# Performance work log

Hardware: AMD Instinct MI355X
Metric: run time of the kernel (lower is better)

The kernel has to match this reference:

```python
import jax, jax.numpy as jnp
import numpy as np

N = 100_000      # nodes
E = 1_600_000    # edges (before self-loops)
IN, OUT, HID = 64, 32, 64
BN_EPS = 1e-5

def _mlp(h, w1, b1, g, beta, w2, b2):
    # PyG MLP (num_layers=2, plain_last=True): Linear -> BatchNorm(train) -> ReLU -> Linear
    h = h @ w1 + b1
    mu = jnp.mean(h, axis=0)
    var = jnp.var(h, axis=0)
    h = (h - mu) * jax.lax.rsqrt(var + BN_EPS) * g + beta
    return jax.nn.relu(h) @ w2 + b2

def setup_inputs() -> dict:
    key = jax.random.key(0)
    ks = jax.random.split(key, 12)
    def rn(k, shape):
        fan_in = shape[0]
        return jax.random.normal(k, shape, jnp.float32) / np.sqrt(fan_in)
    x = jax.random.normal(ks[0], (N, IN), jnp.float32)
    pos = jax.random.normal(ks[1], (N, 3), jnp.float32)
    edge_index = jax.random.randint(ks[2], (2, E), 0, N, jnp.int64)
    return {
        "x": x, "pos": pos, "edge_index": edge_index,
        "w_lin": rn(ks[3], (IN, OUT)), "w_src": rn(ks[4], (IN, OUT)), "w_dst": rn(ks[5], (IN, OUT)),
        "pos_w1": rn(ks[6], (3, HID)), "pos_b1": jnp.zeros((HID,), jnp.float32),
        "pos_g": jnp.ones((HID,), jnp.float32), "pos_beta": jnp.zeros((HID,), jnp.float32),
        "pos_w2": rn(ks[7], (HID, OUT)), "pos_b2": jnp.zeros((OUT,), jnp.float32),
        "att_w1": rn(ks[8], (OUT, HID)), "att_b1": jnp.zeros((HID,), jnp.float32),
        "att_g": jnp.ones((HID,), jnp.float32), "att_beta": jnp.zeros((HID,), jnp.float32),
        "att_w2": rn(ks[9], (HID, OUT)), "att_b2": jnp.zeros((OUT,), jnp.float32),
    }

def reference(x, pos, edge_index, w_lin, w_src, w_dst,
              pos_w1, pos_b1, pos_g, pos_beta, pos_w2, pos_b2,
              att_w1, att_b1, att_g, att_beta, att_w2, att_b2):
    n = x.shape[0]
    # add self-loops (PointTransformerConv default add_self_loops=True)
    loops = jnp.arange(n, dtype=edge_index.dtype)
    src = jnp.concatenate([edge_index[0], loops])  # j (message source)
    dst = jnp.concatenate([edge_index[1], loops])  # i (message target)

    alpha_src = x @ w_src          # [N, OUT]
    alpha_dst = x @ w_dst          # [N, OUT]
    x_val = x @ w_lin              # [N, OUT]

    delta = _mlp(pos[dst] - pos[src], pos_w1, pos_b1, pos_g, pos_beta, pos_w2, pos_b2)  # [E', OUT]
    a = _mlp(alpha_dst[dst] - alpha_src[src] + delta, att_w1, att_b1, att_g, att_beta, att_w2, att_b2)

    # per-destination-node, per-channel softmax over incoming edges
    a_max = jax.ops.segment_max(a, dst, num_segments=n)           # [N, OUT]
    a = jnp.exp(a - a_max[dst])
    denom = jax.ops.segment_sum(a, dst, num_segments=n)           # [N, OUT]
    a = a / (denom[dst] + 1e-16)

    msg = a * (x_val[src] + delta)                                # [E', OUT]
    out = jax.ops.segment_sum(msg, dst, num_segments=n)           # [N, OUT]
    return out
```

## Files before the change

### kernel.cpp

```cpp
#include <hip/hip_runtime.h>

typedef unsigned int uint;
typedef unsigned short ushort;

#define BN_EPS 1e-5f

using bf16x8 = __attribute__((ext_vector_type(8))) short;
using f32x16 = __attribute__((ext_vector_type(16))) float;

union FragU { uint w[4]; bf16x8 v; };

__device__ __forceinline__ uint pk2(float lo, float hi) {
    uint r;
    asm("v_cvt_pk_bf16_f32 %0, %1, %2" : "=v"(r) : "v"(lo), "v"(hi));
    return r;
}
__device__ __forceinline__ float bfu_lo(uint u) { return __uint_as_float(u << 16); }
__device__ __forceinline__ float bfu_hi(uint u) { return __uint_as_float(u & 0xffff0000u); }

__device__ __forceinline__ float upk(const uint* p, int idx) {
    uint u = p[idx >> 1];
    return (idx & 1) ? bfu_hi(u) : bfu_lo(u);
}
__device__ __forceinline__ float upq(const uint2* gq, int r) {
    int g = r >> 2, j = r & 3;
    uint u = (j < 2) ? gq[g].x : gq[g].y;
    return (j & 1) ? bfu_hi(u) : bfu_lo(u);
}

__device__ __forceinline__ void get_rowmap(int col, int* rowv) {
    FragU pa, pb;
    float c = (float)col;
    #pragma unroll
    for (int j = 0; j < 4; j++) { pa.w[j] = pk2(c, c); pb.w[j] = pk2(1.f, 1.f); }
    f32x16 d;
    #pragma unroll
    for (int r = 0; r < 16; r++) d[r] = 0.f;
    d = __builtin_amdgcn_mfma_f32_32x32x16_bf16(pa.v, pb.v, d, 0, 0, 0);
    #pragma unroll
    for (int r = 0; r < 16; r++) {
        int m = (int)(d[r] * 0.0625f + 0.5f);
        rowv[r] = (m < 0) ? 0 : (m > 31 ? 31 : m);
    }
}

template<bool SORTED>
__device__ __forceinline__ void edge_sd(int e, const int* __restrict__ ei,
                                        const int* __restrict__ srcs,
                                        const int* __restrict__ dsts,
                                        int nE, int& src, int& dst) {
    if (SORTED) { src = srcs[e]; dst = dsts[e]; }
    else if (e < nE) { src = ei[e]; dst = ei[nE + e]; }
    else { src = e - nE; dst = src; }
}

__global__ __launch_bounds__(256) void k_node_lin(
    const float* __restrict__ x,
    const float* __restrict__ w_src, const float* __restrict__ w_dst,
    const float* __restrict__ w_lin,
    uint* __restrict__ asx, uint* __restrict__ aDb,
    int nNodes)
{
    int n = blockIdx.x * 256 + threadIdx.x;
    if (n >= nNodes) return;
    float xr[64];
    const float4* xp = (const float4*)(x + (size_t)n * 64);
    #pragma unroll
    for (int i = 0; i < 16; i++) {
        float4 v = xp[i];
        xr[4*i] = v.x; xr[4*i+1] = v.y; xr[4*i+2] = v.z; xr[4*i+3] = v.w;
    }
    const float* ws[3] = { w_src, w_lin, w_dst };
    uint* outs[3] = { asx + (size_t)n*32, asx + (size_t)n*32 + 16, aDb + (size_t)n*16 };
    #pragma unroll
    for (int m = 0; m < 3; m++) {
        const float* w = ws[m];
        float acc[32];
        #pragma unroll
        for (int o = 0; o < 32; o++) acc[o] = 0.f;
        #pragma unroll
        for (int k = 0; k < 64; k++) {
            float xk = xr[k];
            #pragma unroll
            for (int o = 0; o < 32; o++) acc[o] = fmaf(xk, w[k*32+o], acc[o]);
        }
        uint4* op = (uint4*)outs[m];
        #pragma unroll
        for (int q = 0; q < 4; q++) {
            uint4 v;
            v.x = pk2(acc[8*q+0], acc[8*q+1]);
            v.y = pk2(acc[8*q+2], acc[8*q+3]);
            v.z = pk2(acc[8*q+4], acc[8*q+5]);
            v.w = pk2(acc[8*q+6], acc[8*q+7]);
            op[q] = v;
        }
    }
}

__global__ __launch_bounds__(256) void k_pos4(
    const float* __restrict__ pos, float4* __restrict__ pos4, int n)
{
    int i = blockIdx.x * 256 + threadIdx.x;
    if (i < n) pos4[i] = make_float4(pos[i*3], pos[i*3+1], pos[i*3+2], 0.f);
}

__global__ __launch_bounds__(256) void k_hist(
    const int* __restrict__ ei, int* __restrict__ cnt, int nE, int eTot)
{
    int e = blockIdx.x * 256 + threadIdx.x;
    if (e >= eTot) return;
    int dst = (e < nE) ? ei[nE + e] : (e - nE);
    atomicAdd(&cnt[dst], 1);
}

#define SCH 1024
__global__ __launch_bounds__(256) void k_scan1(
    const int* __restrict__ cnt, int* __restrict__ cur,
    int* __restrict__ blkS, int n)
{
    __shared__ int ls[256];
    int t = threadIdx.x;
    int base = blockIdx.x * SCH + t * 4;
    int v0 = (base+0 < n) ? cnt[base+0] : 0;
    int v1 = (base+1 < n) ? cnt[base+1] : 0;
    int v2 = (base+2 < n) ? cnt[base+2] : 0;
    int v3 = (base+3 < n) ? cnt[base+3] : 0;
    int tsum = v0 + v1 + v2 + v3;
    ls[t] = tsum;
    __syncthreads();
    for (int o = 1; o < 256; o <<= 1) {
        int x = (t >= o) ? ls[t-o] : 0;
        __syncthreads();
        ls[t] += x;
        __syncthreads();
    }
    if (t == 255) blkS[blockIdx.x] = ls[255];
    int run = ls[t] - tsum;
    if (base+0 < n) cur[base+0] = run; run += v0;
    if (base+1 < n) cur[base+1] = run; run += v1;
    if (base+2 < n) cur[base+2] = run; run += v2;
    if (base+3 < n) cur[base+3] = run;
}

__global__ void k_scan2(const int* __restrict__ blkS, int* __restrict__ blkOff, int nb)
{
    __shared__ int ls[256];
    int t = threadIdx.x;
    int v = (t < nb) ? blkS[t] : 0;
    ls[t] = v;
    __syncthreads();
    for (int o = 1; o < 256; o <<= 1) {
        int x = (t >= o) ? ls[t-o] : 0;
        __syncthreads();
        ls[t] += x;
        __syncthreads();
    }
    if (t < nb) blkOff[t] = ls[t] - v;
}

__global__ __launch_bounds__(256) void k_scan3(
    int* __restrict__ cur, const int* __restrict__ blkOff, int n)
{
    int off = blkOff[blockIdx.x];
    int base = blockIdx.x * SCH + threadIdx.x * 4;
    #pragma unroll
    for (int j = 0; j < 4; j++) {
        int i = base + j;
        if (i < n) cur[i] += off;
    }
}

__global__ __launch_bounds__(256) void k_rank(
    const int* __restrict__ ei, int* __restrict__ cur,
    int* __restrict__ srcs, int* __restrict__ dsts, int nE, int eTot)
{
    int e = blockIdx.x * 256 + threadIdx.x;
    if (e >= eTot) return;
    int src, dst;
    if (e < nE) { src = ei[e]; dst = ei[nE + e]; }
    else        { src = e - nE; dst = src; }
    int slot = atomicAdd(&cur[dst], 1);
    srcs[slot] = src; dsts[slot] = dst;
}

__global__ __launch_bounds__(256) void k_pos_mom(
    const int* __restrict__ ei, const float4* __restrict__ pos4,
    float* __restrict__ partM, int nE)
{
    float m[9];
    #pragma unroll
    for (int c = 0; c < 9; c++) m[c] = 0.f;
    int stride = gridDim.x * blockDim.x;
    for (int e = blockIdx.x * blockDim.x + threadIdx.x; e < nE; e += stride) {
        int src = ei[e], dst = ei[nE + e];
        float4 pd = pos4[dst], ps = pos4[src];
        float d0 = pd.x - ps.x, d1 = pd.y - ps.y, d2 = pd.z - ps.z;
        m[0] += d0; m[1] += d1; m[2] += d2;
        m[3] = fmaf(d0,d0,m[3]); m[4] = fmaf(d0,d1,m[4]); m[5] = fmaf(d0,d2,m[5]);
        m[6] = fmaf(d1,d1,m[6]); m[7] = fmaf(d1,d2,m[7]); m[8] = fmaf(d2,d2,m[8]);
    }
    __shared__ float red[4][9];
    int w = threadIdx.x >> 6;
    #pragma unroll
    for (int c = 0; c < 9; c++) {
        float t = m[c];
        for (int o = 32; o > 0; o >>= 1) t += __shfl_down(t, o, 64);
        if ((threadIdx.x & 63) == 0) red[w][c] = t;
    }
    __syncthreads();
    if (threadIdx.x < 9)
        partM[blockIdx.x * 9 + threadIdx.x] =
            red[0][threadIdx.x] + red[1][threadIdx.x] + red[2][threadIdx.x] + red[3][threadIdx.x];
}

__global__ void k_bn1_mom(const float* __restrict__ partM, int nBlk,
                          const float* __restrict__ pw1, const float* __restrict__ pb1,
                          const float* __restrict__ g, const float* __restrict__ beta,
                          float* __restrict__ bn, float invE)
{
    __shared__ float mom_s[9];
    int l = threadIdx.x;
    #pragma unroll
    for (int c = 0; c < 9; c++) {
        float s = 0.f;
        for (int i = l; i < nBlk; i += 64) s += partM[i*9 + c];
        for (int o = 32; o > 0; o >>= 1) s += __shfl_down(s, o, 64);
        if (l == 0) mom_s[c] = s;
    }
    __syncthreads();
    int c = l;
    if (c < 64) {
        float w0 = pw1[c], w1 = pw1[64+c], w2 = pw1[128+c], b = pb1[c];
        float S = fmaf(w0, mom_s[0], fmaf(w1, mom_s[1], w2 * mom_s[2]));
        float Q = w0*w0*mom_s[3] + 2.f*w0*w1*mom_s[4] + 2.f*w0*w2*mom_s[5]
                + w1*w1*mom_s[6] + 2.f*w1*w2*mom_s[7] + w2*w2*mom_s[8];
        float mu  = S * invE + b;
        float E2  = Q * invE + 2.f * b * (S * invE) + b * b;
        float var = fmaxf(E2 - mu * mu, 0.f);
        float sc  = rsqrtf(var + BN_EPS) * g[c];
        bn[c]      = sc;
        bn[64+c]   = beta[c] - mu * sc;
    }
}

__global__ __launch_bounds__(256) void k_red_stats(
    const float* __restrict__ partD, float* __restrict__ stats2, int nBlk)
{
    int c = blockIdx.x;
    float s = 0.f;
    for (int i = threadIdx.x; i < nBlk; i += 256) s += partD[(size_t)i*128 + c];
    for (int o = 32; o > 0; o >>= 1) s += __shfl_down(s, o, 64);
    __shared__ float red[4];
    if ((threadIdx.x & 63) == 0) red[threadIdx.x >> 6] = s;
    __syncthreads();
    if (threadIdx.x == 0) stats2[c] = red[0] + red[1] + red[2] + red[3];
}

__global__ void k_bn_fin(const float* __restrict__ stats,
                         const float* __restrict__ g, const float* __restrict__ beta,
                         const float* __restrict__ bias,
                         float* __restrict__ bn, float inv_ep)
{
    int c = threadIdx.x;
    if (c < 64) {
        float b   = bias ? bias[c] : 0.f;
        float m0  = stats[c] * inv_ep;
        float mu  = m0 + b;
        float eq  = stats[64+c] * inv_ep + 2.f*b*m0 + b*b;
        float var = fmaxf(eq - mu * mu, 0.f);
        float sc  = rsqrtf(var + BN_EPS) * g[c];
        bn[c]      = sc;
        bn[64+c]   = beta[c] - mu * sc;
    }
}

__global__ void k_fold1(const float* __restrict__ pw1, const float* __restrict__ pb1,
                        const float* __restrict__ bn1,
                        float* __restrict__ pw1f, float* __restrict__ pb1f)
{
    int i = threadIdx.x;
    if (i < 192) pw1f[i] = pw1[i] * bn1[i & 63];
    if (i < 64)  pb1f[i] = pb1[i] * bn1[i] + bn1[64 + i];
}

__global__ void k_fold2(const float* __restrict__ aw1, const float* __restrict__ ab1,
                        const float* __restrict__ bn2,
                        float* __restrict__ aw1f, float* __restrict__ ab1f)
{
    int i = blockIdx.x * 256 + threadIdx.x;
    if (i < 2048) aw1f[i] = aw1[i] * bn2[i & 63];
    if (i < 64)   ab1f[i] = ab1[i] * bn2[i] + bn2[64 + i];
}

template<bool SORTED>
__global__ __launch_bounds__(256, 2) void k_delta_stats(
    const int* __restrict__ ei, const int* __restrict__ srcs, const int* __restrict__ dsts,
    const float4* __restrict__ pos4,
    const uint* __restrict__ asx, const uint* __restrict__ aDb,
    const float* __restrict__ pw1f, const float* __restrict__ pb1f,
    const float* __restrict__ pw2, const float* __restrict__ pb2,
    const float* __restrict__ aw1,
    float* __restrict__ partD, int nE, int eTot)
{
    const int lane = threadIdx.x & 63;
    const int col  = lane & 31;
    const int h    = lane >> 5;
    const int wid  = threadIdx.x >> 6;

    __shared__ float redS[4][64], redQ[4][64];
    __shared__ uint sbuf[4][1024];
    {
        int w = threadIdx.x >> 6, c = threadIdx.x & 63;
        redS[w][c] = 0.f; redQ[w][c] = 0.f;
    }

    bool quadOK;
    int q2[4];
    FragU fw_pw2[4];
    FragU fw_aw1[2][2];
    uint pb2p[8];
    {
        int rowv[16];
        get_rowmap(col, rowv);
        quadOK = true;
        #pragma unroll
        for (int g = 0; g < 4; g++)
            quadOK = quadOK && (rowv[4*g+1] == rowv[4*g]+1)
                            && (rowv[4*g+2] == rowv[4*g]+2)
                            && (rowv[4*g+3] == rowv[4*g]+3);
        #pragma unroll
        for (int g = 0; g < 4; g++) q2[g] = rowv[4*g] >> 2;
        #pragma unroll
        for (int kt = 0; kt < 4; kt++)
            #pragma unroll
            for (int jw = 0; jw < 4; jw++) {
                int m = 2*jw;
                int c0 = 16*kt + 8*(m>>2) + 4*h + (m&3);
                fw_pw2[kt].w[jw] = pk2(pw2[c0*32 + col], pw2[(c0+1)*32 + col]);
            }
        #pragma unroll
        for (int mt = 0; mt < 2; mt++)
            #pragma unroll
            for (int kt = 0; kt < 2; kt++)
                #pragma unroll
                for (int jw = 0; jw < 4; jw++) {
                    int u0 = rowv[8*kt + 2*jw], u1 = rowv[8*kt + 2*jw + 1];
                    fw_aw1[mt][kt].w[jw] = pk2(aw1[u0*64 + 32*mt + col],
                                               aw1[u1*64 + 32*mt + col]);
                }
        #pragma unroll
        for (int g = 0; g < 8; g++)
            pb2p[g] = pk2(pb2[rowv[2*g]], pb2[rowv[2*g+1]]);
    }

    float sA[32], qA[32];
    #pragma unroll
    for (int i = 0; i < 32; i++) { sA[i] = 0.f; qA[i] = 0.f; }

    const int nT = (eTot + 31) >> 5;
    const int gw = (blockIdx.x << 2) + (threadIdx.x >> 6);
    const int nW = gridDim.x << 2;

    if (quadOK) {
        for (int t = gw; t < nT; t += nW) {
            int e = t*32 + col;
            bool valid = e < eTot;
            int ec = valid ? e : eTot - 1;
            int src, dst;
            edge_sd<SORTED>(ec, ei, srcs, dsts, nE, src, dst);
            #pragma unroll
            for (int it = 0; it < 4; it++) {
                int j  = it*8 + (lane >> 3);
                int sj = __shfl(src, j, 64);
                int w  = lane & 7;
                uint4 v = *(const uint4*)(asx + (size_t)sj*32 + w*4);
                *(uint4*)&sbuf[wid][j*32 + ((w ^ (j & 7)) << 2)] = v;
            }
            float4 ps = pos4[src], pd = pos4[dst];
            uint2 gd2[4];
            {
                const uint* rd = aDb + (size_t)dst*16;
                #pragma unroll
                for (int g = 0; g < 4; g++) gd2[g] = *(const uint2*)(rd + 2*q2[g]);
            }
            float p0 = pd.x - ps.x, p1 = pd.y - ps.y, p2 = pd.z - ps.z;

            FragU ft[4];
            #pragma unroll
            for (int kt = 0; kt < 4; kt++)
                #pragma unroll
                for (int mm = 0; mm < 2; mm++) {
                    int cb = 16*kt + 8*mm + 4*h;
                    float4 w0 = *(const float4*)(pw1f +       cb);
                    float4 w1 = *(const float4*)(pw1f + 64  + cb);
                    float4 w2 = *(const float4*)(pw1f + 128 + cb);
                    float4 bb = *(const float4*)(pb1f + cb);
                    float t0 = fmaxf(fmaf(p0,w0.x, fmaf(p1,w1.x, fmaf(p2,w2.x, bb.x))), 0.f);
                    float t1 = fmaxf(fmaf(p0,w0.y, fmaf(p1,w1.y, fmaf(p2,w2.y, bb.y))), 0.f);
                    float t2 = fmaxf(fmaf(p0,w0.z, fmaf(p1,w1.z, fmaf(p2,w2.z, bb.z))), 0.f);
                    float t3 = fmaxf(fmaf(p0,w0.w, fmaf(p1,w1.w, fmaf(p2,w2.w, bb.w))), 0.f);
                    ft[kt].w[2*mm+0] = pk2(t0, t1);
                    ft[kt].w[2*mm+1] = pk2(t2, t3);
                }
            f32x16 adl;
            #pragma unroll
            for (int r = 0; r < 16; r++) adl[r] = upk(pb2p, r);
            #pragma unroll
            for (int kt = 0; kt < 4; kt++)
                adl = __builtin_amdgcn_mfma_f32_32x32x16_bf16(fw_pw2[kt].v, ft[kt].v, adl, 0, 0, 0);

            uint2 gs2[4];
            #pragma unroll
            for (int g = 0; g < 4; g++) {
                int wq = q2[g] >> 1, hf = (q2[g] & 1) << 1;
                gs2[g] = *(const uint2*)&sbuf[wid][col*32 + ((wq ^ (col & 7)) << 2) + hf];
            }

            FragU fu[2];
            #pragma unroll
            for (int kt = 0; kt < 2; kt++)
                #pragma unroll
                for (int jw = 0; jw < 4; jw++) {
                    int r0 = 8*kt + 2*jw;
                    fu[kt].w[jw] = pk2(adl[r0]   + upq(gd2, r0)   - upq(gs2, r0),
                                       adl[r0+1] + upq(gd2, r0+1) - upq(gs2, r0+1));
                }

            f32x16 ah0, ah1;
            #pragma unroll
            for (int r = 0; r < 16; r++) { ah0[r] = 0.f; ah1[r] = 0.f; }
            #pragma unroll
            for (int kt = 0; kt < 2; kt++) {
                ah0 = __builtin_amdgcn_mfma_f32_32x32x16_bf16(fw_aw1[0][kt].v, fu[kt].v, ah0, 0, 0, 0);
                ah1 = __builtin_amdgcn_mfma_f32_32x32x16_bf16(fw_aw1[1][kt].v, fu[kt].v, ah1, 0, 0, 0);
            }
            if (valid) {
                #pragma unroll
                for (int r = 0; r < 16; r++) {
                    sA[r]    += ah0[r];
                    qA[r]     = fmaf(ah0[r], ah0[r], qA[r]);
                    sA[16+r] += ah1[r];
                    qA[16+r]  = fmaf(ah1[r], ah1[r], qA[16+r]);
                }
            }
        }
    } else {
        int rowv[16];
        get_rowmap(col, rowv);
        for (int t = gw; t < nT; t += nW) {
            int e = t*32 + col;
            bool valid = e < eTot;
            int ec = valid ? e : eTot - 1;
            int src, dst;
            edge_sd<SORTED>(ec, ei, srcs, dsts, nE, src, dst);
            float4 pd = pos4[dst], ps = pos4[src];
            float p0 = pd.x - ps.x, p1 = pd.y - ps.y, p2 = pd.z - ps.z;
            FragU ft[4];
            #pragma unroll
            for (int kt = 0; kt < 4; kt++)
                #pragma unroll
                for (int mm = 0; mm < 2; mm++) {
                    int cb = 16*kt + 8*mm + 4*h;
                    float4 w0 = *(const float4*)(pw1f +       cb);
                    float4 w1 = *(const float4*)(pw1f + 64  + cb);
                    float4 w2 = *(const float4*)(pw1f + 128 + cb);
                    float4 bb = *(const float4*)(pb1f + cb);
                    float t0 = fmaxf(fmaf(p0,w0.x, fmaf(p1,w1.x, fmaf(p2,w2.x, bb.x))), 0.f);
                    float t1 = fmaxf(fmaf(p0,w0.y, fmaf(p1,w1.y, fmaf(p2,w2.y, bb.y))), 0.f);
                    float t2 = fmaxf(fmaf(p0,w0.z, fmaf(p1,w1.z, fmaf(p2,w2.z, bb.z))), 0.f);
                    float t3 = fmaxf(fmaf(p0,w0.w, fmaf(p1,w1.w, fmaf(p2,w2.w, bb.w))), 0.f);
                    ft[kt].w[2*mm+0] = pk2(t0, t1);
                    ft[kt].w[2*mm+1] = pk2(t2, t3);
                }
            f32x16 adl;
            #pragma unroll
            for (int r = 0; r < 16; r++) adl[r] = upk(pb2p, r);
            #pragma unroll
            for (int kt = 0; kt < 4; kt++)
                adl = __builtin_amdgcn_mfma_f32_32x32x16_bf16(fw_pw2[kt].v, ft[kt].v, adl, 0, 0, 0);
            const ushort* rs = (const ushort*)(asx + (size_t)src*32);
            const ushort* rd = (const ushort*)(aDb + (size_t)dst*16);
            FragU fu[2];
            #pragma unroll
            for (int kt = 0; kt < 2; kt++)
                #pragma unroll
                for (int jw = 0; jw < 4; jw++) {
                    int r0 = 8*kt + 2*jw;
                    float u0 = adl[r0]   + __uint_as_float(((uint)rd[rowv[r0]])   << 16)
                                         - __uint_as_float(((uint)rs[rowv[r0]])   << 16);
                    float u1 = adl[r0+1] + __uint_as_float(((uint)rd[rowv[r0+1]]) << 16)
                                         - __uint_as_float(((uint)rs[rowv[r0+1]]) << 16);
                    fu[kt].w[jw] = pk2(u0, u1);
                }
            f32x16 ah0, ah1;
            #pragma unroll
            for (int r = 0; r < 16; r++) { ah0[r] = 0.f; ah1[r] = 0.f; }
            #pragma unroll
            for (int kt = 0; kt < 2; kt++) {
                ah0 = __builtin_amdgcn_mfma_f32_32x32x16_bf16(fw_aw1[0][kt].v, fu[kt].v, ah0, 0, 0, 0);
                ah1 = __builtin_amdgcn_mfma_f32_32x32x16_bf16(fw_aw1[1][kt].v, fu[kt].v, ah1, 0, 0, 0);
            }
            if (valid) {
                #pragma unroll
                for (int r = 0; r < 16; r++) {
                    sA[r]    += ah0[r];
                    qA[r]     = fmaf(ah0[r], ah0[r], qA[r]);
                    sA[16+r] += ah1[r];
                    qA[16+r]  = fmaf(ah1[r], ah1[r], qA[16+r]);
                }
            }
        }
    }

    __syncthreads();
    {
        int rv[16];
        get_rowmap(col, rv);
        int w = threadIdx.x >> 6;
        #pragma unroll
        for (int idx = 0; idx < 32; idx++) {
            float vs = sA[idx], vq = qA[idx];
            for (int off = 16; off > 0; off >>= 1) {
                vs += __shfl_xor(vs, off, 64);
                vq += __shfl_xor(vq, off, 64);
            }
            if ((threadIdx.x & 31) == 0) {
                int mt = idx >> 4, r = idx & 15;
                int c = 32*mt + rv[r];
                redS[w][c] = vs;
                redQ[w][c] = vq;
            }
        }
    }
    __syncthreads();
    if (threadIdx.x < 64) {
        int c = threadIdx.x;
        float S = redS[0][c] + redS[1][c] + redS[2][c] + redS[3][c];
        float Q = redQ[0][c] + redQ[1][c] + redQ[2][c] + redQ[3][c];
        partD[(size_t)blockIdx.x*128 + c]      = S;
        partD[(size_t)blockIdx.x*128 + 64 + c] = Q;
    }
}

template<bool SORTED>
__global__ __launch_bounds__(256, 2) void k_att_agg(
    const int* __restrict__ ei, const int* __restrict__ srcs, const int* __restrict__ dsts,
    const float4* __restrict__ pos4,
    const uint* __restrict__ asx, const uint* __restrict__ aDb,
    const float* __restrict__ pw1f, const float* __restrict__ pb1f,
    const float* __restrict__ pw2, const float* __restrict__ pb2,
    const float* __restrict__ aw1f, const float* __restrict__ ab1f,
    const float* __restrict__ aw2, const float* __restrict__ ab2,
    float* __restrict__ denom, float* __restrict__ outp,
    int nE, int eTot)
{
    const int lane = threadIdx.x & 63;
    const int col  = lane & 31;
    const int h    = lane >> 5;
    const int wid  = threadIdx.x >> 6;

    __shared__ uint sbuf[4][1024];

    bool quadOK;
    int q2[4];
    FragU fw_pw2[4], fw_aw2[4];
    FragU fw_aw1[2][2];
    uint pb2p[8], ab2p[8], ab1p[16];
    {
        int rowv[16];
        get_rowmap(col, rowv);
        quadOK = true;
        #pragma unroll
        for (int g = 0; g < 4; g++)
            quadOK = quadOK && (rowv[4*g+1] == rowv[4*g]+1)
                            && (rowv[4*g+2] == rowv[4*g]+2)
                            && (rowv[4*g+3] == rowv[4*g]+3);
        #pragma unroll
        for (int g = 0; g < 4; g++) q2[g] = rowv[4*g] >> 2;
        #pragma unroll
        for (int kt = 0; kt < 4; kt++)
            #pragma unroll
            for (int jw = 0; jw < 4; jw++) {
                int m = 2*jw;
                int c0 = 16*kt + 8*(m>>2) + 4*h + (m&3);
                fw_pw2[kt].w[jw] = pk2(pw2[c0*32 + col], pw2[(c0+1)*32 + col]);
                int o0 = 32*(kt>>1) + rowv[8*(kt&1) + m];
                int o1 = 32*(kt>>1) + rowv[8*(kt&1) + m + 1];
                fw_aw2[kt].w[jw] = pk2(aw2[o0*32 + col], aw2[o1*32 + col]);
            }
        #pragma unroll
        for (int mt = 0; mt < 2; mt++)
            #pragma unroll
            for (int kt = 0; kt < 2; kt++)
                #pragma unroll
                for (int jw = 0; jw < 4; jw++) {
                    int u0 = rowv[8*kt + 2*jw], u1 = rowv[8*kt + 2*jw + 1];
                    fw_aw1[mt][kt].w[jw] = pk2(aw1f[u0*64 + 32*mt + col],
                                               aw1f[u1*64 + 32*mt + col]);
                }
        #pragma unroll
        for (int g = 0; g < 8; g++) {
            pb2p[g] = pk2(pb2[rowv[2*g]], pb2[rowv[2*g+1]]);
            ab2p[g] = pk2(ab2[rowv[2*g]], ab2[rowv[2*g+1]]);
            ab1p[g]     = pk2(ab1f[rowv[2*g]],      ab1f[rowv[2*g+1]]);
            ab1p[8 + g] = pk2(ab1f[32 + rowv[2*g]], ab1f[32 + rowv[2*g+1]]);
        }
    }

    const int nT = (eTot + 31) >> 5;
    const int gw = (blockIdx.x << 2) + (threadIdx.x >> 6);
    const int nW = gridDim.x << 2;

    if (quadOK) {
        for (int t = gw; t < nT; t += nW) {
            int e = t*32 + col;
            bool valid = e < eTot;
            int ec = valid ? e : eTot - 1;
            int src, dst;
            edge_sd<SORTED>(ec, ei, srcs, dsts, nE, src, dst);
            #pragma unroll
            for (int it = 0; it < 4; it++) {
                int j  = it*8 + (lane >> 3);
                int sj = __shfl(src, j, 64);
                int w  = lane & 7;
                uint4 v = *(const uint4*)(asx + (size_t)sj*32 + w*4);
                *(uint4*)&sbuf[wid][j*32 + ((w ^ (j & 7)) << 2)] = v;
            }
            float4 ps = pos4[src], pd = pos4[dst];
            uint2 gd2[4];
            {
                const uint* rd = aDb + (size_t)dst*16;
                #pragma unroll
                for (int g = 0; g < 4; g++) gd2[g] = *(const uint2*)(rd + 2*q2[g]);
            }
            float p0 = pd.x - ps.x, p1 = pd.y - ps.y, p2 = pd.z - ps.z;

            FragU ft[4];
            #pragma unroll
            for (int kt = 0; kt < 4; kt++)
                #pragma unroll
                for (int mm = 0; mm < 2; mm++) {
                    int cb = 16*kt + 8*mm + 4*h;
                    float4 w0 = *(const float4*)(pw1f +       cb);
                    float4 w1 = *(const float4*)(pw1f + 64  + cb);
                    float4 w2 = *(const float4*)(pw1f + 128 + cb);
                    float4 bb = *(const float4*)(pb1f + cb);
                    float t0 = fmaxf(fmaf(p0,w0.x, fmaf(p1,w1.x, fmaf(p2,w2.x, bb.x))), 0.f);
                    float t1 = fmaxf(fmaf(p0,w0.y, fmaf(p1,w1.y, fmaf(p2,w2.y, bb.y))), 0.f);
                    float t2 = fmaxf(fmaf(p0,w0.z, fmaf(p1,w1.z, fmaf(p2,w2.z, bb.z))), 0.f);
                    float t3 = fmaxf(fmaf(p0,w0.w, fmaf(p1,w1.w, fmaf(p2,w2.w, bb.w))), 0.f);
                    ft[kt].w[2*mm+0] = pk2(t0, t1);
                    ft[kt].w[2*mm+1] = pk2(t2, t3);
                }
            f32x16 adl;
            #pragma unroll
            for (int r = 0; r < 16; r++) adl[r] = upk(pb2p, r);
            #pragma unroll
            for (int kt = 0; kt < 4; kt++)
                adl = __builtin_amdgcn_mfma_f32_32x32x16_bf16(fw_pw2[kt].v, ft[kt].v, adl, 0, 0, 0);

            uint2 gs2[4], gx2[4];
            #pragma unroll
            for (int g = 0; g < 4; g++) {
                int wq = q2[g] >> 1, hf = (q2[g] & 1) << 1;
                gs2[g] = *(const uint2*)&sbuf[wid][col*32 + ((wq ^ (col & 7)) << 2) + hf];
                gx2[g] = *(const uint2*)&sbuf[wid][col*32 + (((4 + wq) ^ (col & 7)) << 2) + hf];
            }

            FragU fu[2];
            #pragma unroll
            for (int kt = 0; kt < 2; kt++)
                #pragma unroll
                for (int jw = 0; jw < 4; jw++) {
                    int r0 = 8*kt + 2*jw;
                    fu[kt].w[jw] = pk2(adl[r0]   + upq(gd2, r0)   - upq(gs2, r0),
                                       adl[r0+1] + upq(gd2, r0+1) - upq(gs2, r0+1));
                }

            f32x16 ah0, ah1;
            #pragma unroll
            for (int r = 0; r < 16; r++) { ah0[r] = upk(ab1p, r); ah1[r] = upk(ab1p, 16 + r); }
            #pragma unroll
            for (int kt = 0; kt < 2; kt++) {
                ah0 = __builtin_amdgcn_mfma_f32_32x32x16_bf16(fw_aw1[0][kt].v, fu[kt].v, ah0, 0, 0, 0);
                ah1 = __builtin_amdgcn_mfma_f32_32x32x16_bf16(fw_aw1[1][kt].v, fu[kt].v, ah1, 0, 0, 0);
            }
            FragU fh[4];
            #pragma unroll
            for (int q = 0; q < 4; q++)
                #pragma unroll
                for (int jw = 0; jw < 4; jw++) {
                    int r0 = 8*(q&1) + 2*jw;
                    float x0 = (q < 2) ? ah0[r0]   : ah1[r0];
                    float x1 = (q < 2) ? ah0[r0+1] : ah1[r0+1];
                    fh[q].w[jw] = pk2(fmaxf(x0, 0.f), fmaxf(x1, 0.f));
                }
            f32x16 aa;
            #pragma unroll
            for (int r = 0; r < 16; r++) aa[r] = upk(ab2p, r);
            aa = __builtin_amdgcn_mfma_f32_32x32x16_bf16(fw_aw2[0].v, fh[0].v, aa, 0, 0, 0);
            aa = __builtin_amdgcn_mfma_f32_32x32x16_bf16(fw_aw2[1].v, fh[1].v, aa, 0, 0, 0);
            aa = __builtin_amdgcn_mfma_f32_32x32x16_bf16(fw_aw2[2].v, fh[2].v, aa, 0, 0, 0);
            aa = __builtin_amdgcn_mfma_f32_32x32x16_bf16(fw_aw2[3].v, fh[3].v, aa, 0, 0, 0);

            if (SORTED) {
                int lw = lane & 31;
                int dprev = __shfl_up(dst, 1, 32);
                bool isHead = (lw == 0) || (dprev != dst);
                bool eq1  = (__shfl_down(dst, 1, 32)  == dst) && (lw + 1  < 32);
                bool eq2  = (__shfl_down(dst, 2, 32)  == dst) && (lw + 2  < 32);
                bool eq4  = (__shfl_down(dst, 4, 32)  == dst) && (lw + 4  < 32);
                bool eq8  = (__shfl_down(dst, 8, 32)  == dst) && (lw + 8  < 32);
                bool eq16 = (__shfl_down(dst, 16, 32) == dst) && (lw + 16 < 32);
                float* drow = denom + (size_t)dst * 32;
                float* orow = outp  + (size_t)dst * 32;
                #pragma unroll
                for (int r = 0; r < 16; r++) {
                    float ea = __expf(fminf(aa[r], 35.f));
                    float ev = valid ? ea : 0.f;
                    float mv = valid ? ea * (upq(gx2, r) + adl[r]) : 0.f;
                    { float a = __shfl_down(ev,1,32),  b = __shfl_down(mv,1,32);  if (eq1)  { ev += a; mv += b; } }
                    { float a = __shfl_down(ev,2,32),  b = __shfl_down(mv,2,32);  if (eq2)  { ev += a; mv += b; } }
                    { float a = __shfl_down(ev,4,32),  b = __shfl_down(mv,4,32);  if (eq4)  { ev += a; mv += b; } }
                    { float a = __shfl_down(ev,8,32),  b = __shfl_down(mv,8,32);  if (eq8)  { ev += a; mv += b; } }
                    { float a = __shfl_down(ev,16,32), b = __shfl_down(mv,16,32); if (eq16) { ev += a; mv += b; } }
                    if (isHead) {
                        int o = 4*q2[r>>2] + (r&3);
                        unsafeAtomicAdd(drow + o, ev);
                        unsafeAtomicAdd(orow + o, mv);
                    }
                }
            } else if (valid) {
                float* drow = denom + (size_t)dst * 32;
                float* orow = outp  + (size_t)dst * 32;
                #pragma unroll
                for (int r = 0; r < 16; r++) {
                    int o = 4*q2[r>>2] + (r&3);
                    float ea = __expf(fminf(aa[r], 35.f));
                    unsafeAtomicAdd(drow + o, ea);
                    unsafeAtomicAdd(orow + o, ea * (upq(gx2, r) + adl[r]));
                }
            }
        }
    } else {
        int rowv[16];
        get_rowmap(col, rowv);
        for (int t = gw; t < nT; t += nW) {
            int e = t*32 + col;
            bool valid = e < eTot;
            int ec = valid ? e : eTot - 1;
            int src, dst;
            edge_sd<SORTED>(ec, ei, srcs, dsts, nE, src, dst);
            float4 pd = pos4[dst], ps = pos4[src];
            float p0 = pd.x - ps.x, p1 = pd.y - ps.y, p2 = pd.z - ps.z;
            FragU ft[4];
            #pragma unroll
            for (int kt = 0; kt < 4; kt++)
                #pragma unroll
                for (int mm = 0; mm < 2; mm++) {
                    int cb = 16*kt + 8*mm + 4*h;
                    float4 w0 = *(const float4*)(pw1f +       cb);
                    float4 w1 = *(const float4*)(pw1f + 64  + cb);
                    float4 w2 = *(const float4*)(pw1f + 128 + cb);
                    float4 bb = *(const float4*)(pb1f + cb);
                    float t0 = fmaxf(fmaf(p0,w0.x, fmaf(p1,w1.x, fmaf(p2,w2.x, bb.x))), 0.f);
                    float t1 = fmaxf(fmaf(p0,w0.y, fmaf(p1,w1.y, fmaf(p2,w2.y, bb.y))), 0.f);
                    float t2 = fmaxf(fmaf(p0,w0.z, fmaf(p1,w1.z, fmaf(p2,w2.z, bb.z))), 0.f);
                    float t3 = fmaxf(fmaf(p0,w0.w, fmaf(p1,w1.w, fmaf(p2,w2.w, bb.w))), 0.f);
                    ft[kt].w[2*mm+0] = pk2(t0, t1);
                    ft[kt].w[2*mm+1] = pk2(t2, t3);
                }
            f32x16 adl;
            #pragma unroll
            for (int r = 0; r < 16; r++) adl[r] = upk(pb2p, r);
            #pragma unroll
            for (int kt = 0; kt < 4; kt++)
                adl = __builtin_amdgcn_mfma_f32_32x32x16_bf16(fw_pw2[kt].v, ft[kt].v, adl, 0, 0, 0);
            const ushort* rs = (const ushort*)(asx + (size_t)src*32);
            const ushort* rd = (const ushort*)(aDb + (size_t)dst*16);
            FragU fu[2];
            float xg[16];
            #pragma unroll
            for (int r = 0; r < 16; r++)
                xg[r] = __uint_as_float(((uint)rs[32 + rowv[r]]) << 16);
            #pragma unroll
            for (int kt = 0; kt < 2; kt++)
                #pragma unroll
                for (int jw = 0; jw < 4; jw++) {
                    int r0 = 8*kt + 2*jw;
                    float u0 = adl[r0]   + __uint_as_float(((uint)rd[rowv[r0]])   << 16)
                                         - __uint_as_float(((uint)rs[rowv[r0]])   << 16);
                    float u1 = adl[r0+1] + __uint_as_float(((uint)rd[rowv[r0+1]]) << 16)
                                         - __uint_as_float(((uint)rs[rowv[r0+1]]) << 16);
                    fu[kt].w[jw] = pk2(u0, u1);
                }
            f32x16 ah0, ah1;
            #pragma unroll
            for (int r = 0; r < 16; r++) { ah0[r] = upk(ab1p, r); ah1[r] = upk(ab1p, 16 + r); }
            #pragma unroll
            for (int kt = 0; kt < 2; kt++) {
                ah0 = __builtin_amdgcn_mfma_f32_32x32x16_bf16(fw_aw1[0][kt].v, fu[kt].v, ah0, 0, 0, 0);
                ah1 = __builtin_amdgcn_mfma_f32_32x32x16_bf16(fw_aw1[1][kt].v, fu[kt].v, ah1, 0, 0, 0);
            }
            FragU fh[4];
            #pragma unroll
            for (int q = 0; q < 4; q++)
                #pragma unroll
                for (int jw = 0; jw < 4; jw++) {
                    int r0 = 8*(q&1) + 2*jw;
                    float x0 = (q < 2) ? ah0[r0]   : ah1[r0];
                    float x1 = (q < 2) ? ah0[r0+1] : ah1[r0+1];
                    fh[q].w[jw] = pk2(fmaxf(x0, 0.f), fmaxf(x1, 0.f));
                }
            f32x16 aa;
            #pragma unroll
            for (int r = 0; r < 16; r++) aa[r] = upk(ab2p, r);
            aa = __builtin_amdgcn_mfma_f32_32x32x16_bf16(fw_aw2[0].v, fh[0].v, aa, 0, 0, 0);
            aa = __builtin_amdgcn_mfma_f32_32x32x16_bf16(fw_aw2[1].v, fh[1].v, aa, 0, 0, 0);
            aa = __builtin_amdgcn_mfma_f32_32x32x16_bf16(fw_aw2[2].v, fh[2].v, aa, 0, 0, 0);
            aa = __builtin_amdgcn_mfma_f32_32x32x16_bf16(fw_aw2[3].v, fh[3].v, aa, 0, 0, 0);
            if (SORTED) {
                int lw = lane & 31;
                int dprev = __shfl_up(dst, 1, 32);
                bool isHead = (lw == 0) || (dprev != dst);
                bool eq1  = (__shfl_down(dst, 1, 32)  == dst) && (lw + 1  < 32);
                bool eq2  = (__shfl_down(dst, 2, 32)  == dst) && (lw + 2  < 32);
                bool eq4  = (__shfl_down(dst, 4, 32)  == dst) && (lw + 4  < 32);
                bool eq8  = (__shfl_down(dst, 8, 32)  == dst) && (lw + 8  < 32);
                bool eq16 = (__shfl_down(dst, 16, 32) == dst) && (lw + 16 < 32);
                float* drow = denom + (size_t)dst * 32;
                float* orow = outp  + (size_t)dst * 32;
                #pragma unroll
                for (int r = 0; r < 16; r++) {
                    float ea = __expf(fminf(aa[r], 35.f));
                    float ev = valid ? ea : 0.f;
                    float mv = valid ? ea * (xg[r] + adl[r]) : 0.f;
                    { float a = __shfl_down(ev,1,32),  b = __shfl_down(mv,1,32);  if (eq1)  { ev += a; mv += b; } }
                    { float a = __shfl_down(ev,2,32),  b = __shfl_down(mv,2,32);  if (eq2)  { ev += a; mv += b; } }
                    { float a = __shfl_down(ev,4,32),  b = __shfl_down(mv,4,32);  if (eq4)  { ev += a; mv += b; } }
                    { float a = __shfl_down(ev,8,32),  b = __shfl_down(mv,8,32);  if (eq8)  { ev += a; mv += b; } }
                    { float a = __shfl_down(ev,16,32), b = __shfl_down(mv,16,32); if (eq16) { ev += a; mv += b; } }
                    if (isHead) {
                        int o = rowv[r];
                        unsafeAtomicAdd(drow + o, ev);
                        unsafeAtomicAdd(orow + o, mv);
                    }
                }
            } else if (valid) {
                float* drow = denom + (size_t)dst * 32;
                float* orow = outp  + (size_t)dst * 32;
                #pragma unroll
                for (int r = 0; r < 16; r++) {
                    int o = rowv[r];
                    float ea = __expf(fminf(aa[r], 35.f));
                    unsafeAtomicAdd(drow + o, ea);
                    unsafeAtomicAdd(orow + o, ea * (xg[r] + adl[r]));
                }
            }
        }
    }
}

__global__ __launch_bounds__(256) void k_norm(
    float* __restrict__ out, const float* __restrict__ denom, int total)
{
    int i = blockIdx.x * 256 + threadIdx.x;
    if (i < total) out[i] = out[i] / (denom[i] + 1e-16f);
}

extern "C" void kernel_launch(void* const* d_in, const int* in_sizes, int n_in,
                              void* d_out, int out_size, void* d_ws, size_t ws_size,
                              hipStream_t stream)
{
    const float* x     = (const float*)d_in[0];
    const float* pos   = (const float*)d_in[1];
    const int*   ei    = (const int*)d_in[2];
    const float* w_lin = (const float*)d_in[3];
    const float* w_src = (const float*)d_in[4];
    const float* w_dst = (const float*)d_in[5];
    const float* pw1   = (const float*)d_in[6];
    const float* pb1   = (const float*)d_in[7];
    const float* pg    = (const float*)d_in[8];
    const float* pbeta = (const float*)d_in[9];
    const float* pw2   = (const float*)d_in[10];
    const float* pb2   = (const float*)d_in[11];
    const float* aw1   = (const float*)d_in[12];
    const float* ab1   = (const float*)d_in[13];
    const float* ag    = (const float*)d_in[14];
    const float* abeta = (const float*)d_in[15];
    const float* aw2   = (const float*)d_in[16];
    const float* ab2   = (const float*)d_in[17];
    float* out = (float*)d_out;

    const int nNodes = in_sizes[0] / 64;
    const int nE     = in_sizes[2] / 2;
    const int eTot   = nE + nNodes;

    const int PMBLK = 1024;
    const int DBLK  = 2048;

    const size_t nF = (size_t)nNodes * 32;
    uint*   asx   = (uint*)d_ws;
    uint*   aDb   = asx + (size_t)nNodes*32;
    float*  pos4  = (float*)(aDb + (size_t)nNodes*16);
    float*  denom = pos4 + (size_t)nNodes*4;
    float*  stats = denom + nF;
    float*  bn1   = stats + 512;
    float*  bn2   = bn1 + 128;
    float*  pw1f  = bn2 + 128;
    float*  pb1f  = pw1f + 192;
    float*  aw1f  = pb1f + 64;
    float*  ab1f  = aw1f + 2048;
    float*  partM = ab1f + 64;
    float*  partD = partM + (size_t)PMBLK*9;
    float*  fend  = partD + (size_t)DBLK*128;

    int* cnt    = (int*)fend;
    int* cur    = cnt + nNodes;
    int* blkS   = cur + nNodes;
    int* blkOff = blkS + 256;
    int* srcs   = blkOff + 256;
    int* dsts   = srcs + eTot;

    size_t need_sorted = ((char*)(dsts + eTot)) - ((char*)d_ws);
    const bool sorted = ws_size >= need_sorted;

    const int nb = (nNodes + SCH - 1) / SCH;

    hipMemsetAsync(out,   0, nF * sizeof(float), stream);
    hipMemsetAsync(denom, 0, nF * sizeof(float), stream);

    k_node_lin<<<(nNodes + 255) / 256, 256, 0, stream>>>(
        x, w_src, w_dst, w_lin, asx, aDb, nNodes);
    k_pos4<<<(nNodes + 255) / 256, 256, 0, stream>>>(pos, (float4*)pos4, nNodes);

    k_pos_mom<<<PMBLK, 256, 0, stream>>>(ei, (const float4*)pos4, partM, nE);
    k_bn1_mom<<<1, 64, 0, stream>>>(partM, PMBLK, pw1, pb1, pg, pbeta, bn1,
                                    1.0f / (float)eTot);
    k_fold1<<<1, 256, 0, stream>>>(pw1, pb1, bn1, pw1f, pb1f);

    if (sorted) {
        hipMemsetAsync(cnt, 0, (size_t)nNodes * sizeof(int), stream);
        k_hist<<<(eTot + 255) / 256, 256, 0, stream>>>(ei, cnt, nE, eTot);
        k_scan1<<<nb, 256, 0, stream>>>(cnt, cur, blkS, nNodes);
        k_scan2<<<1, 256, 0, stream>>>(blkS, blkOff, nb);
        k_scan3<<<nb, 256, 0, stream>>>(cur, blkOff, nNodes);
        k_rank<<<(eTot + 255) / 256, 256, 0, stream>>>(ei, cur, srcs, dsts, nE, eTot);

        k_delta_stats<true><<<DBLK, 256, 0, stream>>>(
            ei, srcs, dsts, (const float4*)pos4, asx, aDb,
            pw1f, pb1f, pw2, pb2, aw1, partD, nE, eTot);
        k_red_stats<<<128, 256, 0, stream>>>(partD, stats + 128, DBLK);
        k_bn_fin<<<1, 64, 0, stream>>>(stats + 128, ag, abeta, ab1, bn2, 1.0f / (float)eTot);
        k_fold2<<<8, 256, 0, stream>>>(aw1, ab1, bn2, aw1f, ab1f);
        k_att_agg<true><<<DBLK, 256, 0, stream>>>(
            ei, srcs, dsts, (const float4*)pos4, asx, aDb,
            pw1f, pb1f, pw2, pb2, aw1f, ab1f, aw2, ab2, denom, out, nE, eTot);
    } else {
        k_delta_stats<false><<<DBLK, 256, 0, stream>>>(
            ei, nullptr, nullptr, (const float4*)pos4, asx, aDb,
            pw1f, pb1f, pw2, pb2, aw1, partD, nE, eTot);
        k_red_stats<<<128, 256, 0, stream>>>(partD, stats + 128, DBLK);
        k_bn_fin<<<1, 64, 0, stream>>>(stats + 128, ag, abeta, ab1, bn2, 1.0f / (float)eTot);
        k_fold2<<<8, 256, 0, stream>>>(aw1, ab1, bn2, aw1f, ab1f);
        k_att_agg<false><<<DBLK, 256, 0, stream>>>(
            ei, nullptr, nullptr, (const float4*)pos4, asx, aDb,
            pw1f, pb1f, pw2, pb2, aw1f, ab1f, aw2, ab2, denom, out, nE, eTot);
    }
    k_norm<<<(((int)nF) + 255) / 256, 256, 0, stream>>>(out, denom, (int)nF);
}
```

Baseline: 852.7 us.

## Assign whole destination segments per wave to drop atomics, memsets and normalize pass

In the sorted path, each wave now gets an edge range aligned to destination-segment boundaries, found by a ballot search over the sorted dst array. Partial sums for a segment that spans several 32-edge chunks are carried in shared memory. Each output row is written once, already divided by the softmax denominator, so the atomics, the zeroing memsets and the separate normalize kernel are no longer needed. The cost is a boundary search per wave and possible load imbalance when segments are long. Nodes with no incoming edges now depend on self-loops to get written, since out is no longer zeroed.

```diff
diff --git a/kernel.cpp b/kernel.cpp
--- a/kernel.cpp
+++ b/kernel.cpp
@@ -44,14 +44,25 @@
     }
 }
 
-template<bool SORTED>
-__device__ __forceinline__ void edge_sd(int e, const int* __restrict__ ei,
-                                        const int* __restrict__ srcs,
-                                        const int* __restrict__ dsts,
-                                        int nE, int& src, int& dst) {
-    if (SORTED) { src = srcs[e]; dst = dsts[e]; }
-    else if (e < nE) { src = ei[e]; dst = ei[nE + e]; }
-    else { src = e - nE; dst = src; }
+__device__ __forceinline__ int adj_boundary(const int* __restrict__ dsts,
+                                            long tgt, int eTot, int lane) {
+    if (tgt <= 0) return 0;
+    if (tgt >= eTot) return eTot;
+    long base = tgt;
+    while (base < eTot) {
+        long e = base + lane;
+        bool head;
+        if (e < eTot) head = (dsts[e] != dsts[e - 1]);
+        else          head = true;
+        unsigned long long m = __ballot(head);
+        if (m) {
+            int fl = __ffsll((long long)m) - 1;
+            long r = base + fl;
+            return (r > eTot) ? eTot : (int)r;
+        }
+        base += 64;
+    }
+    return eTot;
 }
 
 __global__ __launch_bounds__(256) void k_node_lin(
@@ -367,7 +378,9 @@
             bool valid = e < eTot;
             int ec = valid ? e : eTot - 1;
             int src, dst;
-            edge_sd<SORTED>(ec, ei, srcs, dsts, nE, src, dst);
+            if (SORTED) { src = srcs[ec]; dst = dsts[ec]; }
+            else if (ec < nE) { src = ei[ec]; dst = ei[nE + ec]; }
+            else { src = ec - nE; dst = src; }
             #pragma unroll
             for (int it = 0; it < 4; it++) {
                 int j  = it*8 + (lane >> 3);
@@ -452,7 +465,9 @@
             bool valid = e < eTot;
             int ec = valid ? e : eTot - 1;
             int src, dst;
-            edge_sd<SORTED>(ec, ei, srcs, dsts, nE, src, dst);
+            if (SORTED) { src = srcs[ec]; dst = dsts[ec]; }
+            else if (ec < nE) { src = ei[ec]; dst = ei[nE + ec]; }
+            else { src = ec - nE; dst = src; }
             float4 pd = pos4[dst], ps = pos4[src];
             float p0 = pd.x - ps.x, p1 = pd.y - ps.y, p2 = pd.z - ps.z;
             FragU ft[4];
@@ -542,10 +557,232 @@
     }
 }
 
-template<bool SORTED>
-__global__ __launch_bounds__(256, 2) void k_att_agg(
-    const int* __restrict__ ei, const int* __restrict__ srcs, const int* __restrict__ dsts,
+__global__ __launch_bounds__(256, 2) void k_att_run(
+    const int* __restrict__ srcs, const int* __restrict__ dsts,
     const float4* __restrict__ pos4,
+    const uint* __restrict__ asx, const uint* __restrict__ aDb,
+    const float* __restrict__ pw1f, const float* __restrict__ pb1f,
+    const float* __restrict__ pw2, const float* __restrict__ pb2,
+    const float* __restrict__ aw1f, const float* __restrict__ ab1f,
+    const float* __restrict__ aw2, const float* __restrict__ ab2,
+    float* __restrict__ outp, int eTot, int nWaves)
+{
+    const int lane = threadIdx.x & 63;
+    const int col  = lane & 31;
+    const int h    = lane >> 5;
+    const int wid  = threadIdx.x >> 6;
+    const int gwid = blockIdx.x * 4 + wid;
+
+    __shared__ uint sbuf[4][1024];
+    __shared__ int   s_cdst[4][2];
+    __shared__ float s_cD[4][2][16], s_cO[4][2][16];
+
+    bool quadOK;
+    int q2[4];
+    int rowv[16];
+    FragU fw_pw2[4], fw_aw2[4];
+    FragU fw_aw1[2][2];
+    uint pb2p[8], ab2p[8], ab1p[16];
+    {
+        get_rowmap(col, rowv);
+        quadOK = true;
+        #pragma unroll
+        for (int g = 0; g < 4; g++)
+            quadOK = quadOK && (rowv[4*g+1] == rowv[4*g]+1)
+                            && (rowv[4*g+2] == rowv[4*g]+2)
+                            && (rowv[4*g+3] == rowv[4*g]+3);
+        #pragma unroll
+        for (int g = 0; g < 4; g++) q2[g] = rowv[4*g] >> 2;
+        #pragma unroll
+        for (int kt = 0; kt < 4; kt++)
+            #pragma unroll
+            for (int jw = 0; jw < 4; jw++) {
+                int m = 2*jw;
+                int c0 = 16*kt + 8*(m>>2) + 4*h + (m&3);
+                fw_pw2[kt].w[jw] = pk2(pw2[c0*32 + col], pw2[(c0+1)*32 + col]);
+                int o0 = 32*(kt>>1) + rowv[8*(kt&1) + m];
+                int o1 = 32*(kt>>1) + rowv[8*(kt&1) + m + 1];
+                fw_aw2[kt].w[jw] = pk2(aw2[o0*32 + col], aw2[o1*32 + col]);
+            }
+        #pragma unroll
+        for (int mt = 0; mt < 2; mt++)
+            #pragma unroll
+            for (int kt = 0; kt < 2; kt++)
+                #pragma unroll
+                for (int jw = 0; jw < 4; jw++) {
+                    int u0 = rowv[8*kt + 2*jw], u1 = rowv[8*kt + 2*jw + 1];
+                    fw_aw1[mt][kt].w[jw] = pk2(aw1f[u0*64 + 32*mt + col],
+                                               aw1f[u1*64 + 32*mt + col]);
+                }
+        #pragma unroll
+        for (int g = 0; g < 8; g++) {
+            pb2p[g] = pk2(pb2[rowv[2*g]], pb2[rowv[2*g+1]]);
+            ab2p[g] = pk2(ab2[rowv[2*g]], ab2[rowv[2*g+1]]);
+            ab1p[g]     = pk2(ab1f[rowv[2*g]],      ab1f[rowv[2*g+1]]);
+            ab1p[8 + g] = pk2(ab1f[32 + rowv[2*g]], ab1f[32 + rowv[2*g+1]]);
+        }
+    }
+
+    long tgt0 = (long)gwid * (long)eTot / (long)nWaves;
+    long tgt1 = (long)(gwid + 1) * (long)eTot / (long)nWaves;
+    int rs = adj_boundary(dsts, tgt0, eTot, lane);
+    int re = adj_boundary(dsts, tgt1, eTot, lane);
+
+    if ((lane & 31) == 0) s_cdst[wid][h] = -1;
+
+    for (int eb = rs; eb < re; eb += 32) {
+        int e = eb + col;
+        bool valid = e < re;
+        int ec = valid ? e : re - 1;
+        int src = srcs[ec], dst = dsts[ec];
+        #pragma unroll
+        for (int it = 0; it < 4; it++) {
+            int j  = it*8 + (lane >> 3);
+            int sj = __shfl(src, j, 64);
+            int w  = lane & 7;
+            uint4 v = *(const uint4*)(asx + (size_t)sj*32 + w*4);
+            *(uint4*)&sbuf[wid][j*32 + ((w ^ (j & 7)) << 2)] = v;
+        }
+        float4 ps = pos4[src], pd = pos4[dst];
+        float p0 = pd.x - ps.x, p1 = pd.y - ps.y, p2 = pd.z - ps.z;
+
+        FragU ft[4];
+        #pragma unroll
+        for (int kt = 0; kt < 4; kt++)
+            #pragma unroll
+            for (int mm = 0; mm < 2; mm++) {
+                int cb = 16*kt + 8*mm + 4*h;
+                float4 w0 = *(const float4*)(pw1f +       cb);
+                float4 w1 = *(const float4*)(pw1f + 64  + cb);
+                float4 w2 = *(const float4*)(pw1f + 128 + cb);
+                float4 bb = *(const float4*)(pb1f + cb);
+                float t0 = fmaxf(fmaf(p0,w0.x, fmaf(p1,w1.x, fmaf(p2,w2.x, bb.x))), 0.f);
+                float t1 = fmaxf(fmaf(p0,w0.y, fmaf(p1,w1.y, fmaf(p2,w2.y, bb.y))), 0.f);
+                float t2 = fmaxf(fmaf(p0,w0.z, fmaf(p1,w1.z, fmaf(p2,w2.z, bb.z))), 0.f);
+                float t3 = fmaxf(fmaf(p0,w0.w, fmaf(p1,w1.w, fmaf(p2,w2.w, bb.w))), 0.f);
+                ft[kt].w[2*mm+0] = pk2(t0, t1);
+                ft[kt].w[2*mm+1] = pk2(t2, t3);
+            }
+        f32x16 adl;
+        #pragma unroll
+        for (int r = 0; r < 16; r++) adl[r] = upk(pb2p, r);
+        #pragma unroll
+        for (int kt = 0; kt < 4; kt++)
+            adl = __builtin_amdgcn_mfma_f32_32x32x16_bf16(fw_pw2[kt].v, ft[kt].v, adl, 0, 0, 0);
+
+        uint2 gd2[4], gs2[4], gx2[4];
+        {
+            const uint* rd = aDb + (size_t)dst*16;
+            if (quadOK) {
+                #pragma unroll
+                for (int g = 0; g < 4; g++) gd2[g] = *(const uint2*)(rd + 2*q2[g]);
+                #pragma unroll
+                for (int g = 0; g < 4; g++) {
+                    int wq = q2[g] >> 1, hf = (q2[g] & 1) << 1;
+                    gs2[g] = *(const uint2*)&sbuf[wid][col*32 + ((wq ^ (col & 7)) << 2) + hf];
+                    gx2[g] = *(const uint2*)&sbuf[wid][col*32 + (((4 + wq) ^ (col & 7)) << 2) + hf];
+                }
+            } else {
+                const ushort* rdd = (const ushort*)rd;
+                #pragma unroll
+                for (int g = 0; g < 4; g++) {
+                    uint a0, a1, b0, b1, c0, c1;
+                    int i0 = rowv[4*g], i1 = rowv[4*g+1], i2 = rowv[4*g+2], i3 = rowv[4*g+3];
+                    a0 = ((uint)rdd[i0]) | (((uint)rdd[i1]) << 16);
+                    a1 = ((uint)rdd[i2]) | (((uint)rdd[i3]) << 16);
+                    gd2[g].x = a0; gd2[g].y = a1;
+                    #define SRD(ch, outv) { int wq2 = (ch) >> 1; int grp = wq2 >> 2; int off = wq2 & 3; \
+                        uint uu = sbuf[wid][col*32 + ((grp ^ (col & 7)) << 2) + off]; \
+                        outv = ((ch) & 1) ? (uu >> 16) : (uu & 0xffffu); }
+                    uint s0,s1,s2,s3, x0,x1,x2,x3;
+                    SRD(i0, s0) SRD(i1, s1) SRD(i2, s2) SRD(i3, s3)
+                    SRD(32+i0, x0) SRD(32+i1, x1) SRD(32+i2, x2) SRD(32+i3, x3)
+                    #undef SRD
+                    b0 = s0 | (s1 << 16); b1 = s2 | (s3 << 16);
+                    gs2[g].x = b0; gs2[g].y = b1;
+                    c0 = x0 | (x1 << 16); c1 = x2 | (x3 << 16);
+                    gx2[g].x = c0; gx2[g].y = c1;
+                }
+            }
+        }
+
+        FragU fu[2];
+        #pragma unroll
+        for (int kt = 0; kt < 2; kt++)
+            #pragma unroll
+            for (int jw = 0; jw < 4; jw++) {
+                int r0 = 8*kt + 2*jw;
+                fu[kt].w[jw] = pk2(adl[r0]   + upq(gd2, r0)   - upq(gs2, r0),
+                                   adl[r0+1] + upq(gd2, r0+1) - upq(gs2, r0+1));
+            }
+
+        f32x16 ah0, ah1;
+        #pragma unroll
+        for (int r = 0; r < 16; r++) { ah0[r] = upk(ab1p, r); ah1[r] = upk(ab1p, 16 + r); }
+        #pragma unroll
+        for (int kt = 0; kt < 2; kt++) {
+            ah0 = __builtin_amdgcn_mfma_f32_32x32x16_bf16(fw_aw1[0][kt].v, fu[kt].v, ah0, 0, 0, 0);
+            ah1 = __builtin_amdgcn_mfma_f32_32x32x16_bf16(fw_aw1[1][kt].v, fu[kt].v, ah1, 0, 0, 0);
+        }
+        FragU fh[4];
+        #pragma unroll
+        for (int q = 0; q < 4; q++)
+            #pragma unroll
+            for (int jw = 0; jw < 4; jw++) {
+                int r0 = 8*(q&1) + 2*jw;
+                float x0 = (q < 2) ? ah0[r0]   : ah1[r0];
+                float x1 = (q < 2) ? ah0[r0+1] : ah1[r0+1];
+                fh[q].w[jw] = pk2(fmaxf(x0, 0.f), fmaxf(x1, 0.f));
+            }
+        f32x16 aa;
+        #pragma unroll
+        for (int r = 0; r < 16; r++) aa[r] = upk(ab2p, r);
+        aa = __builtin_amdgcn_mfma_f32_32x32x16_bf16(fw_aw2[0].v, fh[0].v, aa, 0, 0, 0);
+        aa = __builtin_amdgcn_mfma_f32_32x32x16_bf16(fw_aw2[1].v, fh[1].v, aa, 0, 0, 0);
+        aa = __builtin_amdgcn_mfma_f32_32x32x16_bf16(fw_aw2[2].v, fh[2].v, aa, 0, 0, 0);
+        aa = __builtin_amdgcn_mfma_f32_32x32x16_bf16(fw_aw2[3].v, fh[3].v, aa, 0, 0, 0);
+
+        int lw = lane & 31;
+        int dprev = __shfl_up(dst, 1, 32);
+        bool isHead = (lw == 0) || (dprev != dst);
+        bool eq1  = (__shfl_down(dst, 1, 32)  == dst) && (lw + 1  < 32);
+        bool eq2  = (__shfl_down(dst, 2, 32)  == dst) && (lw + 2  < 32);
+        bool eq4  = (__shfl_down(dst, 4, 32)  == dst) && (lw + 4  < 32);
+        bool eq8  = (__shfl_down(dst, 8, 32)  == dst) && (lw + 8  < 32);
+        bool eq16 = (__shfl_down(dst, 16, 32) == dst) && (lw + 16 < 32);
+        int d31 = __shfl(dst, 31, 32);
+        int dnext = (eb + 32 < re) ? dsts[eb + 32] : -1;
+        bool cont = (dnext == d31);
+        bool lastSeg = (dst == d31);
+        int cd = s_cdst[wid][h];
+        float* orow = outp + (size_t)dst * 32;
+        #pragma unroll
+        for (int r = 0; r < 16; r++) {
+            float ea = __expf(fminf(aa[r], 35.f));
+            float ev = valid ? ea : 0.f;
+            float mv = valid ? ea * (upq(gx2, r) + adl[r]) : 0.f;
+            { float a = __shfl_down(ev,1,32),  b = __shfl_down(mv,1,32);  if (eq1)  { ev += a; mv += b; } }
+            { float a = __shfl_down(ev,2,32),  b = __shfl_down(mv,2,32);  if (eq2)  { ev += a; mv += b; } }
+            { float a = __shfl_down(ev,4,32),  b = __shfl_down(mv,4,32);  if (eq4)  { ev += a; mv += b; } }
+            { float a = __shfl_down(ev,8,32),  b = __shfl_down(mv,8,32);  if (eq8)  { ev += a; mv += b; } }
+            { float a = __shfl_down(ev,16,32), b = __shfl_down(mv,16,32); if (eq16) { ev += a; mv += b; } }
+            if (lw == 0 && cd == dst) { ev += s_cD[wid][h][r]; mv += s_cO[wid][h][r]; }
+            if (isHead) {
+                if (lastSeg && cont) {
+                    s_cD[wid][h][r] = ev;
+                    s_cO[wid][h][r] = mv;
+                } else {
+                    int o = quadOK ? (4*q2[r>>2] + (r&3)) : rowv[r];
+                    orow[o] = mv / (ev + 1e-16f);
+                }
+            }
+        }
+        if (lw == 0) s_cdst[wid][h] = cont ? d31 : -1;
+    }
+}
+
+__global__ __launch_bounds__(256, 2) void k_att_uns(
+    const int* __restrict__ ei, const float4* __restrict__ pos4,
     const uint* __restrict__ asx, const uint* __restrict__ aDb,
     const float* __restrict__ pw1f, const float* __restrict__ pb1f,
     const float* __restrict__ pw2, const float* __restrict__ pb2,
@@ -557,305 +794,127 @@
     const int lane = threadIdx.x & 63;
     const int col  = lane & 31;
     const int h    = lane >> 5;
-    const int wid  = threadIdx.x >> 6;
-
-    __shared__ uint sbuf[4][1024];
-
-    bool quadOK;
-    int q2[4];
-    FragU fw_pw2[4], fw_aw2[4];
-    FragU fw_aw1[2][2];
+
+    int rowv[16];
+    get_rowmap(col, rowv);
+    FragU fw_pw2[4], fw_aw2[4], fw_aw1[2][2];
     uint pb2p[8], ab2p[8], ab1p[16];
-    {
-        int rowv[16];
-        get_rowmap(col, rowv);
-        quadOK = true;
-        #pragma unroll
-        for (int g = 0; g < 4; g++)
-            quadOK = quadOK && (rowv[4*g+1] == rowv[4*g]+1)
-                            && (rowv[4*g+2] == rowv[4*g]+2)
-                            && (rowv[4*g+3] == rowv[4*g]+3);
-        #pragma unroll
-        for (int g = 0; g < 4; g++) q2[g] = rowv[4*g] >> 2;
-        #pragma unroll
-        for (int kt = 0; kt < 4; kt++)
+    #pragma unroll
+    for (int kt = 0; kt < 4; kt++)
+        #pragma unroll
+        for (int jw = 0; jw < 4; jw++) {
+            int m = 2*jw;
+            int c0 = 16*kt + 8*(m>>2) + 4*h + (m&3);
+            fw_pw2[kt].w[jw] = pk2(pw2[c0*32 + col], pw2[(c0+1)*32 + col]);
+            int o0 = 32*(kt>>1) + rowv[8*(kt&1) + m];
+            int o1 = 32*(kt>>1) + rowv[8*(kt&1) + m + 1];
+            fw_aw2[kt].w[jw] = pk2(aw2[o0*32 + col], aw2[o1*32 + col]);
+        }
+    #pragma unroll
+    for (int mt = 0; mt < 2; mt++)
+        #pragma unroll
+        for (int kt = 0; kt < 2; kt++)
             #pragma unroll
             for (int jw = 0; jw < 4; jw++) {
-                int m = 2*jw;
-                int c0 = 16*kt + 8*(m>>2) + 4*h + (m&3);
-                fw_pw2[kt].w[jw] = pk2(pw2[c0*32 + col], pw2[(c0+1)*32 + col]);
-                int o0 = 32*(kt>>1) + rowv[8*(kt&1) + m];
-                int o1 = 32*(kt>>1) + rowv[8*(kt&1) + m + 1];
-                fw_aw2[kt].w[jw] = pk2(aw2[o0*32 + col], aw2[o1*32 + col]);
-            }
-        #pragma unroll
-        for (int mt = 0; mt < 2; mt++)
-            #pragma unroll
-            for (int kt = 0; kt < 2; kt++)
-                #pragma unroll
-                for (int jw = 0; jw < 4; jw++) {
-                    int u0 = rowv[8*kt + 2*jw], u1 = rowv[8*kt + 2*jw + 1];
-                    fw_aw1[mt][kt].w[jw] = pk2(aw1f[u0*64 + 32*mt + col],
-                                               aw1f[u1*64 + 32*mt + col]);
-                }
-        #pragma unroll
-        for (int g = 0; g < 8; g++) {
-            pb2p[g] = pk2(pb2[rowv[2*g]], pb2[rowv[2*g+1]]);
-            ab2p[g] = pk2(ab2[rowv[2*g]], ab2[rowv[2*g+1]]);
-            ab1p[g]     = pk2(ab1f[rowv[2*g]],      ab1f[rowv[2*g+1]]);
-            ab1p[8 + g] = pk2(ab1f[32 + rowv[2*g]], ab1f[32 + rowv[2*g+1]]);
-        }
+                int u0 = rowv[8*kt + 2*jw], u1 = rowv[8*kt + 2*jw + 1];
+                fw_aw1[mt][kt].w[jw] = pk2(aw1f[u0*64 + 32*mt + col],
+                                           aw1f[u1*64 + 32*mt + col]);
+            }
+    #pragma unroll
+    for (int g = 0; g < 8; g++) {
+        pb2p[g] = pk2(pb2[rowv[2*g]], pb2[rowv[2*g+1]]);
+        ab2p[g] = pk2(ab2[rowv[2*g]], ab2[rowv[2*g+1]]);
+        ab1p[g]     = pk2(ab1f[rowv[2*g]],      ab1f[rowv[2*g+1]]);
+        ab1p[8 + g] = pk2(ab1f[32 + rowv[2*g]], ab1f[32 + rowv[2*g+1]]);
     }
 
     const int nT = (eTot + 31) >> 5;
     const int gw = (blockIdx.x << 2) + (threadIdx.x >> 6);
     const int nW = gridDim.x << 2;
-
-    if (quadOK) {
-        for (int t = gw; t < nT; t += nW) {
-            int e = t*32 + col;
-            bool valid = e < eTot;
-            int ec = valid ? e : eTot - 1;
-            int src, dst;
-            edge_sd<SORTED>(ec, ei, srcs, dsts, nE, src, dst);
-            #pragma unroll
-            for (int it = 0; it < 4; it++) {
-                int j  = it*8 + (lane >> 3);
-                int sj = __shfl(src, j, 64);
-                int w  = lane & 7;
-                uint4 v = *(const uint4*)(asx + (size_t)sj*32 + w*4);
-                *(uint4*)&sbuf[wid][j*32 + ((w ^ (j & 7)) << 2)] = v;
-            }
-            float4 ps = pos4[src], pd = pos4[dst];
-            uint2 gd2[4];
-            {
-                const uint* rd = aDb + (size_t)dst*16;
-                #pragma unroll
-                for (int g = 0; g < 4; g++) gd2[g] = *(const uint2*)(rd + 2*q2[g]);
-            }
-            float p0 = pd.x - ps.x, p1 = pd.y - ps.y, p2 = pd.z - ps.z;
-
-            FragU ft[4];
-            #pragma unroll
-            for (int kt = 0; kt < 4; kt++)
-                #pragma unroll
-                for (int mm = 0; mm < 2; mm++) {
-                    int cb = 16*kt + 8*mm + 4*h;
-                    float4 w0 = *(const float4*)(pw1f +       cb);
-                    float4 w1 = *(const float4*)(pw1f + 64  + cb);
-                    float4 w2 = *(const float4*)(pw1f + 128 + cb);
-                    float4 bb = *(const float4*)(pb1f + cb);
-                    float t0 = fmaxf(fmaf(p0,w0.x, fmaf(p1,w1.x, fmaf(p2,w2.x, bb.x))), 0.f);
-                    float t1 = fmaxf(fmaf(p0,w0.y, fmaf(p1,w1.y, fmaf(p2,w2.y, bb.y))), 0.f);
-                    float t2 = fmaxf(fmaf(p0,w0.z, fmaf(p1,w1.z, fmaf(p2,w2.z, bb.z))), 0.f);
-                    float t3 = fmaxf(fmaf(p0,w0.w, fmaf(p1,w1.w, fmaf(p2,w2.w, bb.w))), 0.f);
-                    ft[kt].w[2*mm+0] = pk2(t0, t1);
-                    ft[kt].w[2*mm+1] = pk2(t2, t3);
-                }
-            f32x16 adl;
-            #pragma unroll
-            for (int r = 0; r < 16; r++) adl[r] = upk(pb2p, r);
-            #pragma unroll
-            for (int kt = 0; kt < 4; kt++)
-                adl = __builtin_amdgcn_mfma_f32_32x32x16_bf16(fw_pw2[kt].v, ft[kt].v, adl, 0, 0, 0);
-
-            uint2 gs2[4], gx2[4];
-            #pragma unroll
-            for (int g = 0; g < 4; g++) {
-                int wq = q2[g] >> 1, hf = (q2[g] & 1) << 1;
-                gs2[g] = *(const uint2*)&sbuf[wid][col*32 + ((wq ^ (col & 7)) << 2) + hf];
-                gx2[g] = *(const uint2*)&sbuf[wid][col*32 + (((4 + wq) ^ (col & 7)) << 2) + hf];
-            }
-
-            FragU fu[2];
-            #pragma unroll
-            for (int kt = 0; kt < 2; kt++)
-                #pragma unroll
-                for (int jw = 0; jw < 4; jw++) {
-                    int r0 = 8*kt + 2*jw;
-                    fu[kt].w[jw] = pk2(adl[r0]   + upq(gd2, r0)   - upq(gs2, r0),
-                                       adl[r0+1] + upq(gd2, r0+1) - upq(gs2, r0+1));
-                }
-
-            f32x16 ah0, ah1;
-            #pragma unroll
-            for (int r = 0; r < 16; r++) { ah0[r] = upk(ab1p, r); ah1[r] = upk(ab1p, 16 + r); }
-            #pragma unroll
-            for (int kt = 0; kt < 2; kt++) {
-                ah0 = __builtin_amdgcn_mfma_f32_32x32x16_bf16(fw_aw1[0][kt].v, fu[kt].v, ah0, 0, 0, 0);
-                ah1 = __builtin_amdgcn_mfma_f32_32x32x16_bf16(fw_aw1[1][kt].v, fu[kt].v, ah1, 0, 0, 0);
-            }
-            FragU fh[4];
-            #pragma unroll
-            for (int q = 0; q < 4; q++)
-                #pragma unroll
-                for (int jw = 0; jw < 4; jw++) {
-                    int r0 = 8*(q&1) + 2*jw;
-                    float x0 = (q < 2) ? ah0[r0]   : ah1[r0];
-                    float x1 = (q < 2) ? ah0[r0+1] : ah1[r0+1];
-                    fh[q].w[jw] = pk2(fmaxf(x0, 0.f), fmaxf(x1, 0.f));
-                }
-            f32x16 aa;
-            #pragma unroll
-            for (int r = 0; r < 16; r++) aa[r] = upk(ab2p, r);
-            aa = __builtin_amdgcn_mfma_f32_32x32x16_bf16(fw_aw2[0].v, fh[0].v, aa, 0, 0, 0);
-            aa = __builtin_amdgcn_mfma_f32_32x32x16_bf16(fw_aw2[1].v, fh[1].v, aa, 0, 0, 0);
-            aa = __builtin_amdgcn_mfma_f32_32x32x16_bf16(fw_aw2[2].v, fh[2].v, aa, 0, 0, 0);
-            aa = __builtin_amdgcn_mfma_f32_32x32x16_bf16(fw_aw2[3].v, fh[3].v, aa, 0, 0, 0);
-
-            if (SORTED) {
-                int lw = lane & 31;
-                int dprev = __shfl_up(dst, 1, 32);
-                bool isHead = (lw == 0) || (dprev != dst);
-                bool eq1  = (__shfl_down(dst, 1, 32)  == dst) && (lw + 1  < 32);
-                bool eq2  = (__shfl_down(dst, 2, 32)  == dst) && (lw + 2  < 32);
-                bool eq4  = (__shfl_down(dst, 4, 32)  == dst) && (lw + 4  < 32);
-                bool eq8  = (__shfl_down(dst, 8, 32)  == dst) && (lw + 8  < 32);
-                bool eq16 = (__shfl_down(dst, 16, 32) == dst) && (lw + 16 < 32);
-                float* drow = denom + (size_t)dst * 32;
-                float* orow = outp  + (size_t)dst * 32;
-                #pragma unroll
-                for (int r = 0; r < 16; r++) {
-                    float ea = __expf(fminf(aa[r], 35.f));
-                    float ev = valid ? ea : 0.f;
-                    float mv = valid ? ea * (upq(gx2, r) + adl[r]) : 0.f;
-                    { float a = __shfl_down(ev,1,32),  b = __shfl_down(mv,1,32);  if (eq1)  { ev += a; mv += b; } }
-                    { float a = __shfl_down(ev,2,32),  b = __shfl_down(mv,2,32);  if (eq2)  { ev += a; mv += b; } }
-                    { float a = __shfl_down(ev,4,32),  b = __shfl_down(mv,4,32);  if (eq4)  { ev += a; mv += b; } }
-                    { float a = __shfl_down(ev,8,32),  b = __shfl_down(mv,8,32);  if (eq8)  { ev += a; mv += b; } }
-                    { float a = __shfl_down(ev,16,32), b = __shfl_down(mv,16,32); if (eq16) { ev += a; mv += b; } }
-                    if (isHead) {
-                        int o = 4*q2[r>>2] + (r&3);
-                        unsafeAtomicAdd(drow + o, ev);
-                        unsafeAtomicAdd(orow + o, mv);
-                    }
-                }
-            } else if (valid) {
-                float* drow = denom + (size_t)dst * 32;
-                float* orow = outp  + (size_t)dst * 32;
-                #pragma unroll
-                for (int r = 0; r < 16; r++) {
-                    int o = 4*q2[r>>2] + (r&3);
-                    float ea = __expf(fminf(aa[r], 35.f));
-                    unsafeAtomicAdd(drow + o, ea);
-                    unsafeAtomicAdd(orow + o, ea * (upq(gx2, r) + adl[r]));
-                }
-            }
-        }
-    } else {
-        int rowv[16];
-        get_rowmap(col, rowv);
-        for (int t = gw; t < nT; t += nW) {
-            int e = t*32 + col;
-            bool valid = e < eTot;
-            int ec = valid ? e : eTot - 1;
-            int src, dst;
-            edge_sd<SORTED>(ec, ei, srcs, dsts, nE, src, dst);
-            float4 pd = pos4[dst], ps = pos4[src];
-            float p0 = pd.x - ps.x, p1 = pd.y - ps.y, p2 = pd.z - ps.z;
-            FragU ft[4];
-            #pragma unroll
-            for (int kt = 0; kt < 4; kt++)
-                #pragma unroll
-                for (int mm = 0; mm < 2; mm++) {
-                    int cb = 16*kt + 8*mm + 4*h;
-                    float4 w0 = *(const float4*)(pw1f +       cb);
-                    float4 w1 = *(const float4*)(pw1f + 64  + cb);
-                    float4 w2 = *(const float4*)(pw1f + 128 + cb);
-                    float4 bb = *(const float4*)(pb1f + cb);
-                    float t0 = fmaxf(fmaf(p0,w0.x, fmaf(p1,w1.x, fmaf(p2,w2.x, bb.x))), 0.f);
-                    float t1 = fmaxf(fmaf(p0,w0.y, fmaf(p1,w1.y, fmaf(p2,w2.y, bb.y))), 0.f);
-                    float t2 = fmaxf(fmaf(p0,w0.z, fmaf(p1,w1.z, fmaf(p2,w2.z, bb.z))), 0.f);
-                    float t3 = fmaxf(fmaf(p0,w0.w, fmaf(p1,w1.w, fmaf(p2,w2.w, bb.w))), 0.f);
-                    ft[kt].w[2*mm+0] = pk2(t0, t1);
-                    ft[kt].w[2*mm+1] = pk2(t2, t3);
-                }
-            f32x16 adl;
-            #pragma unroll
-            for (int r = 0; r < 16; r++) adl[r] = upk(pb2p, r);
-            #pragma unroll
-            for (int kt = 0; kt < 4; kt++)
-                adl = __builtin_amdgcn_mfma_f32_32x32x16_bf16(fw_pw2[kt].v, ft[kt].v, adl, 0, 0, 0);
-            const ushort* rs = (const ushort*)(asx + (size_t)src*32);
-            const ushort* rd = (const ushort*)(aDb + (size_t)dst*16);
-            FragU fu[2];
-            float xg[16];
-            #pragma unroll
-            for (int r = 0; r < 16; r++)
-                xg[r] = __uint_as_float(((uint)rs[32 + rowv[r]]) << 16);
-            #pragma unroll
-            for (int kt = 0; kt < 2; kt++)
-                #pragma unroll
-                for (int jw = 0; jw < 4; jw++) {
-                    int r0 = 8*kt + 2*jw;
-                    float u0 = adl[r0]   + __uint_as_float(((uint)rd[rowv[r0]])   << 16)
-                                         - __uint_as_float(((uint)rs[rowv[r0]])   << 16);
-                    float u1 = adl[r0+1] + __uint_as_float(((uint)rd[rowv[r0+1]]) << 16)
-                                         - __uint_as_float(((uint)rs[rowv[r0+1]]) << 16);
-                    fu[kt].w[jw] = pk2(u0, u1);
-                }
-            f32x16 ah0, ah1;
-            #pragma unroll
-            for (int r = 0; r < 16; r++) { ah0[r] = upk(ab1p, r); ah1[r] = upk(ab1p, 16 + r); }
-            #pragma unroll
-            for (int kt = 0; kt < 2; kt++) {
-                ah0 = __builtin_amdgcn_mfma_f32_32x32x16_bf16(fw_aw1[0][kt].v, fu[kt].v, ah0, 0, 0, 0);
-                ah1 = __builtin_amdgcn_mfma_f32_32x32x16_bf16(fw_aw1[1][kt].v, fu[kt].v, ah1, 0, 0, 0);
-            }
-            FragU fh[4];
-            #pragma unroll
-            for (int q = 0; q < 4; q++)
-                #pragma unroll
-                for (int jw = 0; jw < 4; jw++) {
-                    int r0 = 8*(q&1) + 2*jw;
-                    float x0 = (q < 2) ? ah0[r0]   : ah1[r0];
-                    float x1 = (q < 2) ? ah0[r0+1] : ah1[r0+1];
-                    fh[q].w[jw] = pk2(fmaxf(x0, 0.f), fmaxf(x1, 0.f));
-                }
-            f32x16 aa;
-            #pragma unroll
-            for (int r = 0; r < 16; r++) aa[r] = upk(ab2p, r);
-            aa = __builtin_amdgcn_mfma_f32_32x32x16_bf16(fw_aw2[0].v, fh[0].v, aa, 0, 0, 0);
-            aa = __builtin_amdgcn_mfma_f32_32x32x16_bf16(fw_aw2[1].v, fh[1].v, aa, 0, 0, 0);
-            aa = __builtin_amdgcn_mfma_f32_32x32x16_bf16(fw_aw2[2].v, fh[2].v, aa, 0, 0, 0);
-            aa = __builtin_amdgcn_mfma_f32_32x32x16_bf16(fw_aw2[3].v, fh[3].v, aa, 0, 0, 0);
-            if (SORTED) {
-                int lw = lane & 31;
-                int dprev = __shfl_up(dst, 1, 32);
-                bool isHead = (lw == 0) || (dprev != dst);
-                bool eq1  = (__shfl_down(dst, 1, 32)  == dst) && (lw + 1  < 32);
-                bool eq2  = (__shfl_down(dst, 2, 32)  == dst) && (lw + 2  < 32);
-                bool eq4  = (__shfl_down(dst, 4, 32)  == dst) && (lw + 4  < 32);
-                bool eq8  = (__shfl_down(dst, 8, 32)  == dst) && (lw + 8  < 32);
-                bool eq16 = (__shfl_down(dst, 16, 32) == dst) && (lw + 16 < 32);
-                float* drow = denom + (size_t)dst * 32;
-                float* orow = outp  + (size_t)dst * 32;
-                #pragma unroll
-                for (int r = 0; r < 16; r++) {
-                    float ea = __expf(fminf(aa[r], 35.f));
-                    float ev = valid ? ea : 0.f;
-                    float mv = valid ? ea * (xg[r] + adl[r]) : 0.f;
-                    { float a = __shfl_down(ev,1,32),  b = __shfl_down(mv,1,32);  if (eq1)  { ev += a; mv += b; } }
-                    { float a = __shfl_down(ev,2,32),  b = __shfl_down(mv,2,32);  if (eq2)  { ev += a; mv += b; } }
-                    { float a = __shfl_down(ev,4,32),  b = __shfl_down(mv,4,32);  if (eq4)  { ev += a; mv += b; } }
-                    { float a = __shfl_down(ev,8,32),  b = __shfl_down(mv,8,32);  if (eq8)  { ev += a; mv += b; } }
-                    { float a = __shfl_down(ev,16,32), b = __shfl_down(mv,16,32); if (eq16) { ev += a; mv += b; } }
-                    if (isHead) {
-                        int o = rowv[r];
-                        unsafeAtomicAdd(drow + o, ev);
-                        unsafeAtomicAdd(orow + o, mv);
-                    }
-                }
-            } else if (valid) {
-                float* drow = denom + (size_t)dst * 32;
-                float* orow = outp  + (size_t)dst * 32;
-                #pragma unroll
-                for (int r = 0; r < 16; r++) {
-                    int o = rowv[r];
-                    float ea = __expf(fminf(aa[r], 35.f));
-                    unsafeAtomicAdd(drow + o, ea);
-                    unsafeAtomicAdd(orow + o, ea * (xg[r] + adl[r]));
-                }
+    for (int t = gw; t < nT; t += nW) {
+        int e = t*32 + col;
+        bool valid = e < eTot;
+        int ec = valid ? e : eTot - 1;
+        int src, dst;
+        if (ec < nE) { src = ei[ec]; dst = ei[nE + ec]; }
+        else         { src = ec - nE; dst = src; }
+        float4 pd = pos4[dst], ps = pos4[src];
+        float p0 = pd.x - ps.x, p1 = pd.y - ps.y, p2 = pd.z - ps.z;
+        FragU ft[4];
+        #pragma unroll
+        for (int kt = 0; kt < 4; kt++)
+            #pragma unroll
+            for (int mm = 0; mm < 2; mm++) {
+                int cb = 16*kt + 8*mm + 4*h;
+                float4 w0 = *(const float4*)(pw1f +       cb);
+                float4 w1 = *(const float4*)(pw1f + 64  + cb);
+                float4 w2 = *(const float4*)(pw1f + 128 + cb);
+                float4 bb = *(const float4*)(pb1f + cb);
+                float t0 = fmaxf(fmaf(p0,w0.x, fmaf(p1,w1.x, fmaf(p2,w2.x, bb.x))), 0.f);
+                float t1 = fmaxf(fmaf(p0,w0.y, fmaf(p1,w1.y, fmaf(p2,w2.y, bb.y))), 0.f);
+                float t2 = fmaxf(fmaf(p0,w0.z, fmaf(p1,w1.z, fmaf(p2,w2.z, bb.z))), 0.f);
+                float t3 = fmaxf(fmaf(p0,w0.w, fmaf(p1,w1.w, fmaf(p2,w2.w, bb.w))), 0.f);
+                ft[kt].w[2*mm+0] = pk2(t0, t1);
+                ft[kt].w[2*mm+1] = pk2(t2, t3);
+            }
+        f32x16 adl;
+        #pragma unroll
+        for (int r = 0; r < 16; r++) adl[r] = upk(pb2p, r);
+        #pragma unroll
+        for (int kt = 0; kt < 4; kt++)
+            adl = __builtin_amdgcn_mfma_f32_32x32x16_bf16(fw_pw2[kt].v, ft[kt].v, adl, 0, 0, 0);
+        const ushort* rs = (const ushort*)(asx + (size_t)src*32);
+        const ushort* rd = (const ushort*)(aDb + (size_t)dst*16);
+        float xg[16];
+        #pragma unroll
+        for (int r = 0; r < 16; r++)
+            xg[r] = __uint_as_float(((uint)rs[32 + rowv[r]]) << 16);
+        FragU fu[2];
+        #pragma unroll
+        for (int kt = 0; kt < 2; kt++)
+            #pragma unroll
+            for (int jw = 0; jw < 4; jw++) {
+                int r0 = 8*kt + 2*jw;
+                float u0 = adl[r0]   + __uint_as_float(((uint)rd[rowv[r0]])   << 16)
+                                     - __uint_as_float(((uint)rs[rowv[r0]])   << 16);
+                float u1 = adl[r0+1] + __uint_as_float(((uint)rd[rowv[r0+1]]) << 16)
+                                     - __uint_as_float(((uint)rs[rowv[r0+1]]) << 16);
+                fu[kt].w[jw] = pk2(u0, u1);
+            }
+        f32x16 ah0, ah1;
+        #pragma unroll
+        for (int r = 0; r < 16; r++) { ah0[r] = upk(ab1p, r); ah1[r] = upk(ab1p, 16 + r); }
+        #pragma unroll
+        for (int kt = 0; kt < 2; kt++) {
+            ah0 = __builtin_amdgcn_mfma_f32_32x32x16_bf16(fw_aw1[0][kt].v, fu[kt].v, ah0, 0, 0, 0);
+            ah1 = __builtin_amdgcn_mfma_f32_32x32x16_bf16(fw_aw1[1][kt].v, fu[kt].v, ah1, 0, 0, 0);
+        }
+        FragU fh[4];
+        #pragma unroll
+        for (int q = 0; q < 4; q++)
+            #pragma unroll
+            for (int jw = 0; jw < 4; jw++) {
+                int r0 = 8*(q&1) + 2*jw;
+                float x0 = (q < 2) ? ah0[r0]   : ah1[r0];
+                float x1 = (q < 2) ? ah0[r0+1] : ah1[r0+1];
+                fh[q].w[jw] = pk2(fmaxf(x0, 0.f), fmaxf(x1, 0.f));
+            }
+        f32x16 aa;
+        #pragma unroll
+        for (int r = 0; r < 16; r++) aa[r] = upk(ab2p, r);
+        aa = __builtin_amdgcn_mfma_f32_32x32x16_bf16(fw_aw2[0].v, fh[0].v, aa, 0, 0, 0);
+        aa = __builtin_amdgcn_mfma_f32_32x32x16_bf16(fw_aw2[1].v, fh[1].v, aa, 0, 0, 0);
+        aa = __builtin_amdgcn_mfma_f32_32x32x16_bf16(fw_aw2[2].v, fh[2].v, aa, 0, 0, 0);
+        aa = __builtin_amdgcn_mfma_f32_32x32x16_bf16(fw_aw2[3].v, fh[3].v, aa, 0, 0, 0);
+        if (valid) {
+            float* drow = denom + (size_t)dst * 32;
+            float* orow = outp  + (size_t)dst * 32;
+            #pragma unroll
+            for (int r = 0; r < 16; r++) {
+                int o = rowv[r];
+                float ea = __expf(fminf(aa[r], 35.f));
+                unsafeAtomicAdd(drow + o, ea);
+                unsafeAtomicAdd(orow + o, ea * (xg[r] + adl[r]));
             }
         }
     }
@@ -927,9 +986,6 @@
 
     const int nb = (nNodes + SCH - 1) / SCH;
 
-    hipMemsetAsync(out,   0, nF * sizeof(float), stream);
-    hipMemsetAsync(denom, 0, nF * sizeof(float), stream);
-
     k_node_lin<<<(nNodes + 255) / 256, 256, 0, stream>>>(
         x, w_src, w_dst, w_lin, asx, aDb, nNodes);
     k_pos4<<<(nNodes + 255) / 256, 256, 0, stream>>>(pos, (float4*)pos4, nNodes);
@@ -953,19 +1009,21 @@
         k_red_stats<<<128, 256, 0, stream>>>(partD, stats + 128, DBLK);
         k_bn_fin<<<1, 64, 0, stream>>>(stats + 128, ag, abeta, ab1, bn2, 1.0f / (float)eTot);
         k_fold2<<<8, 256, 0, stream>>>(aw1, ab1, bn2, aw1f, ab1f);
-        k_att_agg<true><<<DBLK, 256, 0, stream>>>(
-            ei, srcs, dsts, (const float4*)pos4, asx, aDb,
-            pw1f, pb1f, pw2, pb2, aw1f, ab1f, aw2, ab2, denom, out, nE, eTot);
+        k_att_run<<<DBLK, 256, 0, stream>>>(
+            srcs, dsts, (const float4*)pos4, asx, aDb,
+            pw1f, pb1f, pw2, pb2, aw1f, ab1f, aw2, ab2, out, eTot, DBLK * 4);
     } else {
+        hipMemsetAsync(out,   0, nF * sizeof(float), stream);
+        hipMemsetAsync(denom, 0, nF * sizeof(float), stream);
         k_delta_stats<false><<<DBLK, 256, 0, stream>>>(
             ei, nullptr, nullptr, (const float4*)pos4, asx, aDb,
             pw1f, pb1f, pw2, pb2, aw1, partD, nE, eTot);
         k_red_stats<<<128, 256, 0, stream>>>(partD, stats + 128, DBLK);
         k_bn_fin<<<1, 64, 0, stream>>>(stats + 128, ag, abeta, ab1, bn2, 1.0f / (float)eTot);
         k_fold2<<<8, 256, 0, stream>>>(aw1, ab1, bn2, aw1f, ab1f);
-        k_att_agg<false><<<DBLK, 256, 0, stream>>>(
-            ei, nullptr, nullptr, (const float4*)pos4, asx, aDb,
+        k_att_uns<<<DBLK, 256, 0, stream>>>(
+            ei, (const float4*)pos4, asx, aDb,
             pw1f, pb1f, pw2, pb2, aw1f, ab1f, aw2, ab2, denom, out, nE, eTot);
-    }
-    k_norm<<<(((int)nF) + 255) / 256, 256, 0, stream>>>(out, denom, (int)nF);
-}
+        k_norm<<<(((int)nF) + 255) / 256, 256, 0, stream>>>(out, denom, (int)nF);
+    }
+}
```

New measurement: 973.5 us. 14.2% more time.
